# Kernel optimization log

Hardware: AMD Instinct MI355X
Metric: run time of the kernel (lower is better)

Reference implementation:

```python
import jax, jax.numpy as jnp
import numpy as np

B, N, D, H = 512, 200, 128, 8
DH = D // H
CLIP = 10.0
NEG = -1e9


def setup_inputs():
    ks = jax.random.split(jax.random.key(0), 10)
    s = 1.0 / float(np.sqrt(D))
    f32 = jnp.float32
    return {
        "x": jax.random.normal(ks[0], (2, B, N, N), f32),
        "rf": jax.random.uniform(ks[1], (B, 2), f32),
        "node_embeddings": jax.random.normal(ks[2], (B, N, D), f32),
        "graph_embedding": jax.random.normal(ks[3], (B, D), f32),
        "Wk1_w": jax.random.normal(ks[4], (D, D), f32) * s,
        "Wk1_b": jnp.zeros((D,), f32),
        "Wv_w": jax.random.normal(ks[5], (D, D), f32) * s,
        "Wk2_w": jax.random.normal(ks[6], (D, D), f32) * s,
        "Wout_w": jax.random.normal(ks[7], (D, D), f32) * s,
        "Wq_w": jax.random.normal(ks[8], (D, D + 2), f32) * s,
        "init_node": jnp.zeros((D,), f32),
    }


def _forward(x, rf, node_embeddings, Wk1_w, Wk1_b, Wv_w, Wk2_w, Wout_w, Wq_w, init_node):
    # static projections (compute_static)
    K1 = node_embeddings @ Wk1_w.T + Wk1_b  # [B,N,D]
    V = node_embeddings @ Wv_w.T
    K2 = node_embeddings @ Wk2_w.T
    K1h = K1.reshape(B, N, H, DH).transpose(0, 2, 1, 3)  # [B,H,N,DH]
    Vh = V.reshape(B, N, H, DH).transpose(0, 2, 1, 3)
    barange = jnp.arange(B)
    narange = jnp.arange(N)

    def step(carry, _):
        mask, ctx, end = carry  # mask [B,N] bool, ctx [B,2+D], end [B] bool
        Q1 = ctx @ Wq_w.T  # [B,D]  (Wq_step)
        qh = Q1.reshape(B, H, DH)
        scores = jnp.einsum('bhd,bhnd->bhn', qh, K1h) / jnp.sqrt(jnp.float32(DH))
        scores = jnp.where(mask[:, None, :], NEG, scores)
        attn = jax.nn.softmax(scores, axis=-1)
        mha = jnp.einsum('bhn,bhnd->bhd', attn, Vh).reshape(B, D)
        Q2 = mha @ Wout_w.T  # [B,D]
        logits = CLIP * jnp.tanh(jnp.einsum('bd,bnd->bn', Q2, K2) / jnp.sqrt(jnp.float32(D)))
        logits = jnp.where(mask, NEG, logits)
        log_p = jax.nn.log_softmax(logits, axis=-1)  # [B,N]
        nxt = jnp.argmax(log_p, axis=-1)  # greedy decode (deterministic)
        nxt = jnp.where(end, nxt, 0)  # once node 0 chosen, stay at 0
        cur_emb = node_embeddings[barange, nxt]  # [B,D]
        end = end & (nxt != 0)
        mask = mask | (narange[None, :] == nxt[:, None])
        ctx = jnp.concatenate([rf, cur_emb], axis=1)
        return (mask, ctx, end), (log_p, nxt)

    ctx0 = jnp.concatenate([rf, jnp.broadcast_to(init_node, (B, D))], axis=1)
    carry0 = (jnp.zeros((B, N), bool), ctx0, jnp.ones((B,), bool))
    _, (log_ps, tours) = jax.lax.scan(step, carry0, None, length=N)
    log_ps = log_ps.transpose(1, 0, 2)  # [B,N,N]
    pi = tours.T  # [B,N]

    # get_cost
    index = jnp.argmax(pi == 0, axis=1)  # first occurrence of stop node 0
    steps_mask = narange[None, :] < index[:, None]
    cols = pi * steps_mask
    sol = jnp.zeros((B, N), jnp.float32).at[barange[:, None], cols].set(1.0)
    f1 = jnp.einsum('bn,bnm,bm->b', sol, x[0], sol)[:, None, None]  # [B,1,1]
    f2 = jnp.einsum('bn,bnm,bm->b', sol, x[1], sol)[:, None, None]
    cost = -(f1 * rf[0, 0] + f2 * rf[0, 1]).squeeze()  # [B]

    # log-likelihood of tour, weighted by solution membership
    chosen = jnp.take_along_axis(log_ps, pi[:, :, None], axis=2)[:, :, 0]  # [B,N]
    w = jnp.take_along_axis(sol, pi, axis=1)
    ll = jnp.sum(chosen * w, axis=1)  # [B]
    return cost, f1, f2, ll, pi


def reference(x, rf, node_embeddings, graph_embedding, Wk1_w, Wk1_b, Wv_w, Wk2_w, Wout_w, Wq_w, init_node):
    return _forward(x, rf, node_embeddings, Wk1_w, Wk1_b, Wv_w, Wk2_w, Wout_w, Wq_w, init_node)
```

## Files before the change

kernel.cpp:

```cpp
#include <hip/hip_runtime.h>
#include <math.h>

#define NEGV (-1e9f)

#define OUT_F   0l
#define M_F     52428800l
#define QR_F    (M_F + 65536l)
#define QI_F    (QR_F + 65536l)
#define SOL_F   (QI_F + 65536l)
#define WS_FLOATS (SOL_F + 102400l)

typedef float f32x4 __attribute__((ext_vector_type(4)));

#define DPPF(x, ctrl, oldv) __int_as_float(__builtin_amdgcn_update_dpp( \
      __float_as_int(oldv), __float_as_int(x), ctrl, 0xF, 0xF, false))

__device__ __forceinline__ float wave_max(float x) {
  x = fmaxf(x, DPPF(x, 0x111, -INFINITY));
  x = fmaxf(x, DPPF(x, 0x112, -INFINITY));
  x = fmaxf(x, DPPF(x, 0x114, -INFINITY));
  x = fmaxf(x, DPPF(x, 0x118, -INFINITY));
  x = fmaxf(x, DPPF(x, 0x142, -INFINITY));
  x = fmaxf(x, DPPF(x, 0x143, -INFINITY));
  return __int_as_float(__builtin_amdgcn_readlane(__float_as_int(x), 63));
}
__device__ __forceinline__ float wave_sum(float x) {
  x = x + DPPF(x, 0x111, 0.f);
  x = x + DPPF(x, 0x112, 0.f);
  x = x + DPPF(x, 0x114, 0.f);
  x = x + DPPF(x, 0x118, 0.f);
  x = x + DPPF(x, 0x142, 0.f);
  x = x + DPPF(x, 0x143, 0.f);
  return __int_as_float(__builtin_amdgcn_readlane(__float_as_int(x), 63));
}

__global__ __launch_bounds__(256)
void build_M(const float* __restrict__ Wk1, const float* __restrict__ Wv,
             const float* __restrict__ Wk2, const float* __restrict__ Wout,
             const float* __restrict__ Wq, float* __restrict__ Mbuf) {
  int g = blockIdx.x * 256 + threadIdx.x;
  int j = g >> 9, c = g & 511;
  float val;
  if (c < 128) {
    val = Wk1[c * 128 + j];
  } else if (c < 256) {
    val = Wv[(c - 128) * 128 + j];
  } else if (c < 384) {
    int d = c - 256;
    float s = 0.f;
    for (int e = 0; e < 128; ++e) s += Wk2[e * 128 + j] * Wout[e * 128 + d];
    val = s;
  } else {
    val = Wq[(c - 384) * 130 + 2 + j];
  }
  Mbuf[j * 512 + c] = val;
}

__global__ __launch_bounds__(256)
void build_Q(const float* __restrict__ rf, const float* __restrict__ Wq,
             const float* __restrict__ initn, float* __restrict__ QR,
             float* __restrict__ QI) {
  int g = blockIdx.x * 256 + threadIdx.x;
  int b = g >> 7, d = g & 127;
  float qr = Wq[d * 130 + 0] * rf[b * 2 + 0] + Wq[d * 130 + 1] * rf[b * 2 + 1];
  float qi = qr;
  for (int j = 0; j < 128; ++j) qi += Wq[d * 130 + 2 + j] * initn[j];
  QR[g] = qr;
  QI[g] = qi;
}

__global__ __launch_bounds__(256)
void gemm_static(const float* __restrict__ emb, const float* __restrict__ Mbuf,
                 const float* __restrict__ bk1, const float* __restrict__ QR,
                 float* __restrict__ OUT) {
  int bid = blockIdx.x;
  int rt = bid >> 3, ct = bid & 7;
  int r0 = rt * 64, c0 = ct * 64;
  int t = threadIdx.x, ty = t >> 4, tx = t & 15;
  int row0 = r0 + ty * 4;
  int col  = c0 + tx * 4;
  float acc[4][4] = {};
  const float* mp = Mbuf + col;
  for (int kb = 0; kb < 32; ++kb) {
    int k = kb * 4;
    float4 b0 = *(const float4*)(mp + (long)(k + 0) * 512);
    float4 b1 = *(const float4*)(mp + (long)(k + 1) * 512);
    float4 b2 = *(const float4*)(mp + (long)(k + 2) * 512);
    float4 b3 = *(const float4*)(mp + (long)(k + 3) * 512);
    float bm[4][4] = {{b0.x,b0.y,b0.z,b0.w},{b1.x,b1.y,b1.z,b1.w},
                      {b2.x,b2.y,b2.z,b2.w},{b3.x,b3.y,b3.z,b3.w}};
    #pragma unroll
    for (int rr = 0; rr < 4; ++rr) {
      float4 a4 = *(const float4*)(emb + (long)(row0 + rr) * 128 + k);
      float av[4] = {a4.x, a4.y, a4.z, a4.w};
      #pragma unroll
      for (int i = 0; i < 4; ++i)
        #pragma unroll
        for (int cc = 0; cc < 4; ++cc)
          acc[rr][cc] += av[i] * bm[i][cc];
    }
  }
  float badd[4] = {0.f, 0.f, 0.f, 0.f};
  if (c0 < 128) {
    #pragma unroll
    for (int cc = 0; cc < 4; ++cc) badd[cc] = bk1[col + cc];
  }
  #pragma unroll
  for (int rr = 0; rr < 4; ++rr) {
    int row = row0 + rr;
    float v[4];
    #pragma unroll
    for (int cc = 0; cc < 4; ++cc) v[cc] = acc[rr][cc] + badd[cc];
    if (col >= 384) {
      int bb = row / 200;
      #pragma unroll
      for (int cc = 0; cc < 4; ++cc) v[cc] += QR[bb * 128 + (col - 384) + cc];
    }
    float4 v4; v4.x = v[0]; v4.y = v[1]; v4.z = v[2]; v4.w = v[3];
    *(float4*)(OUT + (long)row * 512 + col) = v4;
  }
}

__global__ void init_ctr(int* __restrict__ c) { *c = 0; }

__global__ __attribute__((amdgpu_flat_work_group_size(512, 512), amdgpu_waves_per_eu(2, 2)))
void decode512(const float* __restrict__ OUT, const float* __restrict__ QI,
               int* __restrict__ ctr, float* __restrict__ sol,
               float* __restrict__ out) {
  __shared__ float sc[1600];
  __shared__ __align__(16) float mhal[128];
  __shared__ float lg[200];
  __shared__ __align__(16) float qv[128];
  __shared__ int bci, bsel;

  const int t = threadIdx.x;
  const int lane = t & 63, wave = t >> 6;
  const int o = t >> 2, r4 = t & 3;
  const int mn = t >> 1, half = t & 1;
  const int vst  = (r4 == 0) ? 0 : (r4 == 1 ? 48 : (r4 == 2 ? 100 : 152));
  const bool mid = (r4 == 1) || (r4 == 2);

  float kreg[64], ureg[64], vreg[52];

  for (;;) {
    if (t == 0) bsel = atomicAdd(ctr, 1);
    __syncthreads();
    const int b = bsel;
    if (b >= 512) break;
    const float* outb = OUT + (long)b * 200 * 512;

    if (t < 400) {
      const float* kp = outb + mn * 512 + 64 * half;
      const float* up = outb + mn * 512 + 256 + 64 * half;
      #pragma unroll
      for (int c = 0; c < 16; ++c)
        *(f32x4*)&kreg[c * 4] = *(const f32x4*)(kp + c * 4);
      #pragma unroll
      for (int c = 0; c < 16; ++c)
        *(f32x4*)&ureg[c * 4] = *(const f32x4*)(up + c * 4);
    }
    {
      const float* vp = outb + 128 + o;
      #pragma unroll
      for (int i = 0; i < 48; ++i) vreg[i] = vp[(vst + i) * 512];
      vreg[48] = mid ? vp[(vst + 48) * 512] : 0.f;
      vreg[49] = mid ? vp[(vst + 49) * 512] : 0.f;
      vreg[50] = mid ? vp[(vst + 50) * 512] : 0.f;
      vreg[51] = mid ? vp[(vst + 51) * 512] : 0.f;
    }
    if (t < 128) qv[t] = QI[b * 128 + t];

    bool cmb = false;
    bool live = true, picked0 = false;
    float llsum = 0.f, chose = 0.f;

    __syncthreads();

    for (int st = 0; st < 200; ++st) {
      if (t < 400) {
        #pragma unroll
        for (int hh = 0; hh < 4; ++hh) {
          float s = 0.f;
          #pragma unroll
          for (int c = 0; c < 4; ++c) {
            f32x4 q4 = *(const f32x4*)&qv[64 * half + hh * 16 + c * 4];
            s += q4[0] * kreg[hh * 16 + c * 4 + 0];
            s += q4[1] * kreg[hh * 16 + c * 4 + 1];
            s += q4[2] * kreg[hh * 16 + c * 4 + 2];
            s += q4[3] * kreg[hh * 16 + c * 4 + 3];
          }
          sc[(4 * half + hh) * 200 + mn] = cmb ? NEGV : s * 0.25f;
        }
      }
      __syncthreads();

      {
        float sv[4];
        float mx = -INFINITY;
        #pragma unroll
        for (int k = 0; k < 4; ++k) {
          int n = lane + 64 * k;
          float s = (n < 200) ? sc[wave * 200 + n] : -INFINITY;
          sv[k] = s;
          mx = fmaxf(mx, s);
        }
        float vmax = wave_max(mx);
        float ls = 0.f;
        #pragma unroll
        for (int k = 0; k < 4; ++k) { sv[k] = expf(sv[k] - vmax); ls += sv[k]; }
        ls = wave_sum(ls);
        #pragma unroll
        for (int k = 0; k < 4; ++k) {
          int n = lane + 64 * k;
          if (n < 200) sc[wave * 200 + n] = sv[k] / ls;
        }
      }
      __syncthreads();

      {
        const float* ap = sc + wave * 200 + vst;
        float a = 0.f;
        #pragma unroll
        for (int c = 0; c < 12; ++c) {
          f32x4 av = *(const f32x4*)(ap + c * 4);
          a += av[0] * vreg[c * 4 + 0];
          a += av[1] * vreg[c * 4 + 1];
          a += av[2] * vreg[c * 4 + 2];
          a += av[3] * vreg[c * 4 + 3];
        }
        if (mid) {
          f32x4 av = *(const f32x4*)(ap + 48);
          a += av[0] * vreg[48]; a += av[1] * vreg[49];
          a += av[2] * vreg[50]; a += av[3] * vreg[51];
        }
        a += DPPF(a, 0xB1, 0.f);
        a += DPPF(a, 0x4E, 0.f);
        if (r4 == 0) mhal[o] = a;
      }
      __syncthreads();

      if (t < 400) {
        float a = 0.f;
        #pragma unroll
        for (int c = 0; c < 16; ++c) {
          f32x4 mh = *(const f32x4*)&mhal[64 * half + c * 4];
          a += mh[0] * ureg[c * 4 + 0];
          a += mh[1] * ureg[c * 4 + 1];
          a += mh[2] * ureg[c * 4 + 2];
          a += mh[3] * ureg[c * 4 + 3];
        }
        a += DPPF(a, 0xB1, 0.f);
        if (half == 0) {
          float l = 10.f * tanhf(a / 11.313708498984761f);
          lg[mn] = cmb ? NEGV : l;
        }
      }
      __syncthreads();

      {
        float lv[4];
        float mx = -INFINITY;
        #pragma unroll
        for (int k = 0; k < 4; ++k) {
          int n = lane + 64 * k;
          lv[k] = (n < 200) ? lg[n] : -INFINITY;
          mx = fmaxf(mx, lv[k]);
        }
        float vmax = wave_max(mx);
        int bidx = -1;
        #pragma unroll
        for (int k = 0; k < 4; ++k) {
          unsigned long long bm =
              __ballot((lane + 64 * k < 200) && (lv[k] == vmax));
          if (bidx < 0 && bm != 0ull) bidx = k * 64 + (int)__builtin_ctzll(bm);
        }
        int nxt = live ? bidx : 0;
        if (t < 128) qv[t] = outb[(long)nxt * 512 + 384 + t];
        float e = 0.f;
        #pragma unroll
        for (int k = 0; k < 4; ++k) e += expf(lv[k] - vmax);
        float se_ = wave_sum(e);
        float lse = logf(se_);
        if (t == 0) {
          chose = live ? (-lse) : ((lv[0] - vmax) - lse);
          out[2048 + (long)b * 200 + st] = (float)nxt;
          bci = nxt;
        }
      }
      __syncthreads();

      int nxt = bci;
      if (!live) {
        if (t == 0) llsum += chose * (float)(200 - st);
        for (int s2 = st + 1 + t; s2 < 200; s2 += 512)
          out[2048 + (long)b * 200 + s2] = 0.f;
        break;
      }
      if (t == 0) llsum += chose;
      if (t < 400 && nxt == mn) cmb = true;
      if (nxt == 0) { live = false; picked0 = true; }
    }

    if (t == 0) out[1536 + b] = picked0 ? llsum : 0.f;
    if (t < 400 && half == 0) {
      float s = (mn == 0) ? 1.f : ((picked0 && cmb) ? 1.f : 0.f);
      sol[(long)b * 200 + mn] = s;
    }
    __syncthreads();
  }
}

__global__ __attribute__((amdgpu_flat_work_group_size(1024, 1024)))
void decode(const float* __restrict__ OUT, const float* __restrict__ QI,
            int* __restrict__ ctr, float* __restrict__ sol,
            float* __restrict__ out) {
  __shared__ __align__(16) float k1r[25600];
  __shared__ __align__(16) float at[1600];
  __shared__ __align__(16) float mhal[128];
  __shared__ float lg[200];
  __shared__ __align__(16) float qv[128];
  __shared__ __align__(16) float ul[12800];
  __shared__ int   bci;
  __shared__ int   bsel;

  const int t = threadIdx.x;
  const int lane = t & 63, wave = t >> 6;
  const int o = t >> 3, q8 = t & 7;
  const int m4 = t >> 2, j4 = t & 3;
  const int stq = (q8 * 25) & ~3;
  const int cq  = ((((q8 + 1) * 25) & ~3) - stq) >> 2;

  for (;;) {
    if (t == 0) bsel = atomicAdd(ctr, 1);
    __syncthreads();
    const int b = bsel;
    if (b >= 512) break;
    const float* outb = OUT + (long)b * 200 * 512;

    for (int p = 0; p < 25; ++p) {
      int f = p * 1024 + t;
      int n = f >> 7, d = f & 127;
      k1r[n * 128 + ((d + 4 * n) & 127)] = outb[n * 512 + d];
    }
    for (int f = t; f < 12800; f += 1024) {
      int m = f >> 6, c = f & 63;
      ul[m * 64 + ((c + 4 * m) & 63)] =
          outb[m * 512 + 256 + (c >> 4) * 32 + 16 + (c & 15)];
    }
    f32x4 vA = {}, vB = {}, vC = {}, vD = {}, vE = {}, vF = {}, vG = {};
    {
      const float* vp = outb + 128 + o;
      #pragma unroll
      for (int e = 0; e < 4; ++e) vA[e] = vp[(stq + 0 + e) * 512];
      #pragma unroll
      for (int e = 0; e < 4; ++e) vB[e] = vp[(stq + 4 + e) * 512];
      #pragma unroll
      for (int e = 0; e < 4; ++e) vC[e] = vp[(stq + 8 + e) * 512];
      #pragma unroll
      for (int e = 0; e < 4; ++e) vD[e] = vp[(stq + 12 + e) * 512];
      #pragma unroll
      for (int e = 0; e < 4; ++e) vE[e] = vp[(stq + 16 + e) * 512];
      #pragma unroll
      for (int e = 0; e < 4; ++e) vF[e] = vp[(stq + 20 + e) * 512];
      if (cq == 7) {
        #pragma unroll
        for (int e = 0; e < 4; ++e) vG[e] = vp[(stq + 24 + e) * 512];
      }
    }
    f32x4 urR0 = {}, urR1 = {}, urR2 = {}, urR3 = {};
    if (t < 800) {
      const float* up = outb + m4 * 512 + 256 + j4 * 32;
      urR0 = *(const f32x4*)(up + 4 * ((0 + j4) & 3));
      urR1 = *(const f32x4*)(up + 4 * ((1 + j4) & 3));
      urR2 = *(const f32x4*)(up + 4 * ((2 + j4) & 3));
      urR3 = *(const f32x4*)(up + 4 * ((3 + j4) & 3));
    }
    if (t < 128) qv[t] = QI[b * 128 + t];

    int mk = 0;
    bool cm = false;
    bool live = true, picked0 = false;
    float llsum = 0.f, chose = 0.f;

    __syncthreads();

    for (int st = 0; st < 200; ++st) {
      if (wave < 8) {
        const int hb = wave * 16;
        float acc[4] = {};
        #pragma unroll
        for (int hf = 0; hf < 2; ++hf) {
          f32x4 qa = *(const f32x4*)&qv[hb + hf * 8];
          f32x4 qb2 = *(const f32x4*)&qv[hb + hf * 8 + 4];
          #pragma unroll
          for (int k = 0; k < 4; ++k) {
            int n = lane + 64 * k;
            if (n < 200) {
              const float* kb = k1r + n * 128;
              int off  = (hb + hf * 8 + 4 * n) & 127;
              int off2 = (hb + hf * 8 + 4 + 4 * n) & 127;
              f32x4 kA = *(const f32x4*)(kb + off);
              f32x4 kB = *(const f32x4*)(kb + off2);
              float ah = qa[0] * kA[0];
              ah += qa[1] * kA[1]; ah += qa[2] * kA[2]; ah += qa[3] * kA[3];
              ah += qb2[0] * kB[0]; ah += qb2[1] * kB[1];
              ah += qb2[2] * kB[2]; ah += qb2[3] * kB[3];
              acc[k] += ah;
            }
          }
        }
        float sv[4];
        float mx = -INFINITY;
        #pragma unroll
        for (int k = 0; k < 4; ++k) {
          int n = lane + 64 * k;
          float s = -INFINITY;
          if (n < 200) {
            s = acc[k] * 0.25f;
            if (mk & (1 << k)) s = NEGV;
          }
          sv[k] = s;
          mx = fmaxf(mx, s);
        }
        float vmax = wave_max(mx);
        float ls = 0.f;
        #pragma unroll
        for (int k = 0; k < 4; ++k) { sv[k] = expf(sv[k] - vmax); ls += sv[k]; }
        ls = wave_sum(ls);
        #pragma unroll
        for (int k = 0; k < 4; ++k) {
          int n = lane + 64 * k;
          if (n < 200) at[wave * 200 + n] = sv[k] / ls;
        }
      }
      __syncthreads();

      {
        const int h2 = t >> 7;
        const float* ap = at + h2 * 200 + stq;
        float a = 0.f;
        f32x4 av;
        av = *(const f32x4*)(ap + 0);
        a += av[0]*vA[0]; a += av[1]*vA[1]; a += av[2]*vA[2]; a += av[3]*vA[3];
        av = *(const f32x4*)(ap + 4);
        a += av[0]*vB[0]; a += av[1]*vB[1]; a += av[2]*vB[2]; a += av[3]*vB[3];
        av = *(const f32x4*)(ap + 8);
        a += av[0]*vC[0]; a += av[1]*vC[1]; a += av[2]*vC[2]; a += av[3]*vC[3];
        av = *(const f32x4*)(ap + 12);
        a += av[0]*vD[0]; a += av[1]*vD[1]; a += av[2]*vD[2]; a += av[3]*vD[3];
        av = *(const f32x4*)(ap + 16);
        a += av[0]*vE[0]; a += av[1]*vE[1]; a += av[2]*vE[2]; a += av[3]*vE[3];
        av = *(const f32x4*)(ap + 20);
        a += av[0]*vF[0]; a += av[1]*vF[1]; a += av[2]*vF[2]; a += av[3]*vF[3];
        if (cq == 7) {
          av = *(const f32x4*)(ap + 24);
          a += av[0]*vG[0]; a += av[1]*vG[1]; a += av[2]*vG[2]; a += av[3]*vG[3];
        }
        a += DPPF(a, 0xB1, 0.f);
        a += DPPF(a, 0x4E, 0.f);
        a += DPPF(a, 0x141, 0.f);
        if (q8 == 0) mhal[o] = a;
      }
      __syncthreads();

      if (t < 800) {
        float a = 0.f;
        {
          f32x4 ml;
          ml = *(const f32x4*)&mhal[j4 * 32 + ((0 + j4) & 3) * 4];
          a += ml[0]*urR0[0]; a += ml[1]*urR0[1]; a += ml[2]*urR0[2]; a += ml[3]*urR0[3];
          ml = *(const f32x4*)&mhal[j4 * 32 + ((1 + j4) & 3) * 4];
          a += ml[0]*urR1[0]; a += ml[1]*urR1[1]; a += ml[2]*urR1[2]; a += ml[3]*urR1[3];
          ml = *(const f32x4*)&mhal[j4 * 32 + ((2 + j4) & 3) * 4];
          a += ml[0]*urR2[0]; a += ml[1]*urR2[1]; a += ml[2]*urR2[2]; a += ml[3]*urR2[3];
          ml = *(const f32x4*)&mhal[j4 * 32 + ((3 + j4) & 3) * 4];
          a += ml[0]*urR3[0]; a += ml[1]*urR3[1]; a += ml[2]*urR3[2]; a += ml[3]*urR3[3];
        }
        const int ubase = m4 * 64;
        #pragma unroll
        for (int c = 0; c < 4; ++c) {
          int ci = (c + j4) & 3;
          f32x4 mh = *(const f32x4*)&mhal[j4 * 32 + 16 + ci * 4];
          f32x4 uu = *(const f32x4*)&ul[ubase + ((j4 * 16 + ci * 4 + 4 * m4) & 63)];
          a += mh[0]*uu[0]; a += mh[1]*uu[1]; a += mh[2]*uu[2]; a += mh[3]*uu[3];
        }
        a += DPPF(a, 0xB1, 0.f);
        a += DPPF(a, 0x4E, 0.f);
        if (j4 == 0) {
          float l = 10.f * tanhf(a / 11.313708498984761f);
          lg[m4] = cm ? NEGV : l;
        }
      }
      __syncthreads();

      if (wave < 8) {
        float lv[4];
        float mx = -INFINITY;
        #pragma unroll
        for (int k = 0; k < 4; ++k) {
          int n = lane + 64 * k;
          lv[k] = (n < 200) ? lg[n] : -INFINITY;
          mx = fmaxf(mx, lv[k]);
        }
        float vmax = wave_max(mx);
        int bidx = -1;
        #pragma unroll
        for (int k = 0; k < 4; ++k) {
          unsigned long long bm =
              __ballot((lane + 64 * k < 200) && (lv[k] == vmax));
          if (bidx < 0 && bm != 0ull) bidx = k * 64 + (int)__builtin_ctzll(bm);
        }
        int nxt = live ? bidx : 0;
        if (t < 128) qv[t] = outb[(long)nxt * 512 + 384 + t];
        float e = 0.f;
        #pragma unroll
        for (int k = 0; k < 4; ++k) e += expf(lv[k] - vmax);
        float se_ = wave_sum(e);
        float lse = logf(se_);
        if (t == 0) {
          chose = live ? (-lse) : ((lv[0] - vmax) - lse);
          out[2048 + (long)b * 200 + st] = (float)nxt;
          bci = nxt;
        }
      }
      __syncthreads();

      int nxt = bci;
      if (!live) {
        if (t == 0) llsum += chose * (float)(200 - st);
        for (int s2 = st + 1 + t; s2 < 200; s2 += 1024)
          out[2048 + (long)b * 200 + s2] = 0.f;
        break;
      }
      if (t == 0) llsum += chose;
      if (wave < 8 && (nxt & 63) == lane) mk |= 1 << (nxt >> 6);
      if (t < 800 && nxt == m4) cm = true;
      if (nxt == 0) { live = false; picked0 = true; }
    }

    if (t == 0) out[1536 + b] = picked0 ? llsum : 0.f;
    if (t < 800 && j4 == 0) {
      float s = (m4 == 0) ? 1.f : ((picked0 && cm) ? 1.f : 0.f);
      sol[(long)b * 200 + m4] = s;
    }
    __syncthreads();
  }
}

__global__ __launch_bounds__(256)
void cost_kernel(const float* __restrict__ x, const float* __restrict__ rf,
                 const float* __restrict__ sol, float* __restrict__ out) {
  __shared__ float solL[256];
  __shared__ float red[8];
  const int b = blockIdx.x, t = threadIdx.x;
  solL[t] = (t < 200) ? sol[b * 200 + t] : 0.f;
  __syncthreads();
  const float* x0 = x + (long)b * 40000;
  const float* x1 = x + 20480000l + (long)b * 40000;
  float a1 = 0.f, a2 = 0.f;
  if (t < 200) {
    for (int i = 0; i < 200; ++i) {
      if (solL[i] != 0.f) {
        a1 += x0[i * 200 + t];
        a2 += x1[i * 200 + t];
      }
    }
    float w = solL[t];
    a1 *= w; a2 *= w;
  }
  #pragma unroll
  for (int off = 32; off > 0; off >>= 1) {
    a1 += __shfl_xor(a1, off);
    a2 += __shfl_xor(a2, off);
  }
  if ((t & 63) == 0) { red[(t >> 6) * 2] = a1; red[(t >> 6) * 2 + 1] = a2; }
  __syncthreads();
  if (t == 0) {
    float f1 = red[0] + red[2] + red[4] + red[6];
    float f2 = red[1] + red[3] + red[5] + red[7];
    out[b]        = -(f1 * rf[0] + f2 * rf[1]);
    out[512 + b]  = f1;
    out[1024 + b] = f2;
  }
}

extern "C" void kernel_launch(void* const* d_in, const int* in_sizes, int n_in,
                              void* d_out, int out_size, void* d_ws, size_t ws_size,
                              hipStream_t stream) {
  const float* x     = (const float*)d_in[0];
  const float* rf    = (const float*)d_in[1];
  const float* emb   = (const float*)d_in[2];
  const float* Wk1   = (const float*)d_in[4];
  const float* bk1   = (const float*)d_in[5];
  const float* Wv    = (const float*)d_in[6];
  const float* Wk2   = (const float*)d_in[7];
  const float* Wout  = (const float*)d_in[8];
  const float* Wq    = (const float*)d_in[9];
  const float* initn = (const float*)d_in[10];
  float* out = (float*)d_out;
  float* ws  = (float*)d_ws;

  if (ws_size < (size_t)WS_FLOATS * 4) return;

  float* OUTb = ws + OUT_F;
  float* Mb   = ws + M_F;
  float* QRb  = ws + QR_F;
  float* QIb  = ws + QI_F;
  float* solb = ws + SOL_F;

  build_M<<<256, 256, 0, stream>>>(Wk1, Wv, Wk2, Wout, Wq, Mb);
  build_Q<<<256, 256, 0, stream>>>(rf, Wq, initn, QRb, QIb);
  gemm_static<<<12800, 256, 0, stream>>>(emb, Mb, bk1, QRb, OUTb);
  init_ctr<<<1, 1, 0, stream>>>((int*)QRb);

  hipFuncAttributes fa;
  bool big = false;
  if (hipFuncGetAttributes(&fa, (const void*)decode512) == hipSuccess)
    big = (fa.numRegs >= 160);
  if (big)
    decode512<<<256, 512, 0, stream>>>(OUTb, QIb, (int*)QRb, solb, out);
  else
    decode<<<256, 1024, 0, stream>>>(OUTb, QIb, (int*)QRb, solb, out);

  cost_kernel<<<512, 256, 0, stream>>>(x, rf, solb, out);
}
```

Baseline: 1.426 ms.

## Preload all query rows into LDS and split dot-product accumulators

```diff
diff --git a/kernel.cpp b/kernel.cpp
--- a/kernel.cpp
+++ b/kernel.cpp
@@ -127,10 +127,10 @@
 void decode512(const float* __restrict__ OUT, const float* __restrict__ QI,
                int* __restrict__ ctr, float* __restrict__ sol,
                float* __restrict__ out) {
+  __shared__ __align__(16) float qall[201 * 128];
   __shared__ float sc[1600];
   __shared__ __align__(16) float mhal[128];
   __shared__ float lg[200];
-  __shared__ __align__(16) float qv[128];
   __shared__ int bci, bsel;
 
   const int t = threadIdx.x;
@@ -149,6 +149,10 @@
     if (b >= 512) break;
     const float* outb = OUT + (long)b * 200 * 512;
 
+    for (int f = t; f < 25728; f += 512) {
+      int row = f >> 7, d = f & 127;
+      qall[f] = (row < 200) ? outb[row * 512 + 384 + d] : QI[b * 128 + d];
+    }
     if (t < 400) {
       const float* kp = outb + mn * 512 + 64 * half;
       const float* up = outb + mn * 512 + 256 + 64 * half;
@@ -168,8 +172,8 @@
       vreg[50] = mid ? vp[(vst + 50) * 512] : 0.f;
       vreg[51] = mid ? vp[(vst + 51) * 512] : 0.f;
     }
-    if (t < 128) qv[t] = QI[b * 128 + t];
-
+
+    int cur = 200;
     bool cmb = false;
     bool live = true, picked0 = false;
     float llsum = 0.f, chose = 0.f;
@@ -178,12 +182,13 @@
 
     for (int st = 0; st < 200; ++st) {
       if (t < 400) {
+        const float* qb = qall + cur * 128 + 64 * half;
         #pragma unroll
         for (int hh = 0; hh < 4; ++hh) {
           float s = 0.f;
           #pragma unroll
           for (int c = 0; c < 4; ++c) {
-            f32x4 q4 = *(const f32x4*)&qv[64 * half + hh * 16 + c * 4];
+            f32x4 q4 = *(const f32x4*)(qb + hh * 16 + c * 4);
             s += q4[0] * kreg[hh * 16 + c * 4 + 0];
             s += q4[1] * kreg[hh * 16 + c * 4 + 1];
             s += q4[2] * kreg[hh * 16 + c * 4 + 2];
@@ -219,20 +224,23 @@
 
       {
         const float* ap = sc + wave * 200 + vst;
-        float a = 0.f;
+        float ac[4] = {0.f, 0.f, 0.f, 0.f};
         #pragma unroll
         for (int c = 0; c < 12; ++c) {
           f32x4 av = *(const f32x4*)(ap + c * 4);
-          a += av[0] * vreg[c * 4 + 0];
-          a += av[1] * vreg[c * 4 + 1];
-          a += av[2] * vreg[c * 4 + 2];
-          a += av[3] * vreg[c * 4 + 3];
+          float s = av[0] * vreg[c * 4 + 0];
+          s += av[1] * vreg[c * 4 + 1];
+          s += av[2] * vreg[c * 4 + 2];
+          s += av[3] * vreg[c * 4 + 3];
+          ac[c & 3] += s;
         }
         if (mid) {
           f32x4 av = *(const f32x4*)(ap + 48);
-          a += av[0] * vreg[48]; a += av[1] * vreg[49];
-          a += av[2] * vreg[50]; a += av[3] * vreg[51];
-        }
+          float s = av[0] * vreg[48];
+          s += av[1] * vreg[49]; s += av[2] * vreg[50]; s += av[3] * vreg[51];
+          ac[0] += s;
+        }
+        float a = (ac[0] + ac[1]) + (ac[2] + ac[3]);
         a += DPPF(a, 0xB1, 0.f);
         a += DPPF(a, 0x4E, 0.f);
         if (r4 == 0) mhal[o] = a;
@@ -240,15 +248,17 @@
       __syncthreads();
 
       if (t < 400) {
-        float a = 0.f;
+        float ac[4] = {0.f, 0.f, 0.f, 0.f};
         #pragma unroll
         for (int c = 0; c < 16; ++c) {
           f32x4 mh = *(const f32x4*)&mhal[64 * half + c * 4];
-          a += mh[0] * ureg[c * 4 + 0];
-          a += mh[1] * ureg[c * 4 + 1];
-          a += mh[2] * ureg[c * 4 + 2];
-          a += mh[3] * ureg[c * 4 + 3];
-        }
+          float s = mh[0] * ureg[c * 4 + 0];
+          s += mh[1] * ureg[c * 4 + 1];
+          s += mh[2] * ureg[c * 4 + 2];
+          s += mh[3] * ureg[c * 4 + 3];
+          ac[c & 3] += s;
+        }
+        float a = (ac[0] + ac[1]) + (ac[2] + ac[3]);
         a += DPPF(a, 0xB1, 0.f);
         if (half == 0) {
           float l = 10.f * tanhf(a / 11.313708498984761f);
@@ -275,7 +285,6 @@
           if (bidx < 0 && bm != 0ull) bidx = k * 64 + (int)__builtin_ctzll(bm);
         }
         int nxt = live ? bidx : 0;
-        if (t < 128) qv[t] = outb[(long)nxt * 512 + 384 + t];
         float e = 0.f;
         #pragma unroll
         for (int k = 0; k < 4; ++k) e += expf(lv[k] - vmax);
@@ -298,6 +307,7 @@
       }
       if (t == 0) llsum += chose;
       if (t < 400 && nxt == mn) cmb = true;
+      cur = nxt;
       if (nxt == 0) { live = false; picked0 = true; }
     }
 
@@ -616,7 +626,7 @@
   hipFuncAttributes fa;
   bool big = false;
   if (hipFuncGetAttributes(&fa, (const void*)decode512) == hipSuccess)
-    big = (fa.numRegs >= 160);
+    big = (fa.localSizeBytes <= 64);
   if (big)
     decode512<<<256, 512, 0, stream>>>(OUTb, QIb, (int*)QRb, solb, out);
   else
```

Measured after the change: 1.393 ms. -2.3%, faster.
